# Kernel optimization log

Measured on AMD Instinct MI355X. Metric: run time of the kernel, lower is better.

## Reference

```python
import jax, jax.numpy as jnp
import numpy as np

NUM_COMPONENTS = 8
STRIDE, PADDING, OUTPUT_PADDING, K = 2, 1, 0, 4


def get_comp_mat(n):
    # Cayley-Dickson construction: entry [i, j] = +/- component index of the
    # weight multiplying input component j to produce output component i.
    A = np.array([[0]])
    while A.shape[0] < n:
        m = A.shape[0]
        A = np.vstack([np.hstack([A, -(A + m)]), np.hstack([A + m, A])])
    return A


def setup_inputs() -> dict:
    key = jax.random.key(0)
    k1, k2, k3 = jax.random.split(key, 3)
    B, Cin, Cout, H = 8, 512, 256, 64
    c_in, c_out = Cin // NUM_COMPONENTS, Cout // NUM_COMPONENTS
    x = jax.random.normal(k1, (B, Cin, H, H), jnp.float32)
    # per-component ConvTranspose2d weights, torch layout [C_in, C_out, kH, kW]
    W = jax.random.normal(k2, (NUM_COMPONENTS, c_in, c_out, K, K), jnp.float32) * 0.05
    b = jax.random.normal(k3, (NUM_COMPONENTS, c_out), jnp.float32) * 0.05
    return {"x": x, "W": W, "b": b}


def reference(x, W, b):
    n = NUM_COMPONENTS
    comp = get_comp_mat(n)                 # static [n, n] signed component table
    signs = jnp.asarray(np.where(comp < 0, -1.0, 1.0), x.dtype)
    idx = np.abs(comp)                     # which sub-conv weight to use
    c_in, c_out, kh, kw = W.shape[1:]
    # Fuse the n^2 transpose convs into ONE block transpose conv:
    # Kbig[j*c_in:(j+1)*c_in, i*c_out:(i+1)*c_out] = sign[i,j] * W[idx[i,j]]
    Wsel = W[idx] * signs[:, :, None, None, None, None]          # [ni, nj, c_in, c_out, kh, kw]
    Wbig = jnp.transpose(Wsel, (1, 2, 0, 3, 4, 5)).reshape(n * c_in, n * c_out, kh, kw)
    bbig = jnp.einsum('ij,ijc->ic', signs, b[idx]).reshape(n * c_out)
    # torch ConvTranspose2d == conv with input dilated by stride and flipped kernel
    rhs = jnp.flip(Wbig, (2, 3)).transpose(1, 0, 2, 3)           # OIHW
    pad = K - 1 - PADDING
    out = jax.lax.conv_general_dilated(
        x, rhs, window_strides=(1, 1),
        padding=((pad, pad + OUTPUT_PADDING), (pad, pad + OUTPUT_PADDING)),
        lhs_dilation=(STRIDE, STRIDE),
        dimension_numbers=('NCHW', 'OIHW', 'NCHW'))
    return out + bbig[None, :, None, None]
```

## Files before the change

### kernel.cpp

```cpp
#include <hip/hip_runtime.h>
#include <hip/hip_bf16.h>

typedef unsigned short ushort_t;
typedef __attribute__((ext_vector_type(8))) short short8;
typedef __attribute__((ext_vector_type(4))) float f32x4;

#define NCOMP    8
#define CIN      512
#define COUT     256
#define H        64
#define HP       66
#define OHW      128
#define NB       8

__device__ const int d_idx8[8][8] = {
    {0,1,2,1,4,3,2,3},
    {1,0,3,2,5,4,1,2},
    {2,1,0,1,6,5,4,3},
    {3,2,1,0,7,6,5,4},
    {4,3,2,3,0,1,2,1},
    {5,4,1,2,1,0,3,2},
    {6,5,4,3,2,1,0,1},
    {7,6,5,4,3,2,1,0}};

__device__ const int kh_tab[2][2] = {{1,3},{0,2}};
__device__ const int dh_tab[2][2] = {{0,-1},{1,0}};

__global__ void zero_halo(ushort_t* __restrict__ xpadT) {
    const int t = blockIdx.x * 256 + threadIdx.x;
    const int nA = 8 * 2 * 66 * 64;
    short8 z = {0, 0, 0, 0, 0, 0, 0, 0};
    if (t < nA) {
        int v  = t & 63;
        int r  = t >> 6;
        int iw = r % 66;
        int q  = r / 66;
        int ih = (q & 1) * 65;
        int b  = q >> 1;
        *(short8*)(xpadT + (((size_t)b * HP + ih) * HP + iw) * CIN + v * 8) = z;
    } else {
        int u  = t - nA;
        int v  = u & 63;
        int r  = u >> 6;
        int e  = r & 1;
        int q  = r >> 1;
        int ih = (q & 63) + 1;
        int b  = q >> 6;
        int iw = e * 65;
        *(short8*)(xpadT + (((size_t)b * HP + ih) * HP + iw) * CIN + v * 8) = z;
    }
}

__global__ void prep_x(const float* __restrict__ x, ushort_t* __restrict__ xpadT) {
    __shared__ ushort_t tile[32][33];
    const int ih  = blockIdx.x;
    const int iw0 = (blockIdx.y & 1) * 32;
    const int ic0 = (blockIdx.y >> 1) * 32;
    const int b   = blockIdx.z;
    const int t   = threadIdx.x;

    for (int e = t; e < 1024; e += 256) {
        int icl = e >> 5, iwl = e & 31;
        float v = x[(((size_t)b * CIN + ic0 + icl) * H + ih) * H + iw0 + iwl];
        __hip_bfloat16 h = __float2bfloat16(v);
        tile[icl][iwl] = *(ushort_t*)&h;
    }
    __syncthreads();
    const int iwl = t >> 3, g = t & 7;
    ushort4 v;
    v.x = tile[g * 4 + 0][iwl];
    v.y = tile[g * 4 + 1][iwl];
    v.z = tile[g * 4 + 2][iwl];
    v.w = tile[g * 4 + 3][iwl];
    ushort_t* dst = xpadT + (((size_t)b * HP + ih + 1) * HP + iw0 + iwl + 1) * CIN + ic0 + g * 4;
    *(ushort4*)dst = v;
}

__global__ void prep_w(const float* __restrict__ W, const float* __restrict__ bias,
                       ushort_t* __restrict__ Abf, float* __restrict__ bbig) {
    const int t = blockIdx.x * blockDim.x + threadIdx.x;
    if (t < 4 * 64 * 256 * 32) {
        int kin = t & 31;
        int oc  = (t >> 5) & 255;
        int ks  = (t >> 13) & 63;
        int cls = t >> 19;
        int k  = ks * 32 + kin;
        int a  = k >> 10, c = (k >> 9) & 1, ic = k & 511;
        int ph = cls >> 1, pw = cls & 1;
        int kh = kh_tab[ph][a], kw = kh_tab[pw][c];
        int i = oc >> 5, co = oc & 31;
        int j = ic >> 6, ci = ic & 63;
        float s = (i >= j) ? 1.0f : -1.0f;
        float v = s * W[(((size_t)(d_idx8[i][j] * 64 + ci) * 32 + co) * 4 + kh) * 4 + kw];
        __hip_bfloat16 h = __float2bfloat16(v);
        Abf[t] = *(ushort_t*)&h;
    }
    if (t < COUT) {
        int i = t >> 5, co = t & 31;
        float acc = 0.0f;
        for (int j = 0; j < NCOMP; ++j)
            acc += ((i >= j) ? 1.0f : -1.0f) * bias[d_idx8[i][j] * 32 + co];
        bbig[t] = acc;
    }
}

__device__ __forceinline__ void async16(void* lds_dst, const void* g_src) {
    __builtin_amdgcn_global_load_lds(
        (const __attribute__((address_space(1))) unsigned int*)g_src,
        (__attribute__((address_space(3))) unsigned int*)lds_dst,
        16, 0, 0);
}

#define STAGE(NS, CB)                                                          \
  {                                                                            \
    const int ns_  = (NS);                                                     \
    const int na_  = ns_ >> 5;                                                 \
    const int ncb_ = (ns_ >> 4) & 1;                                           \
    const int go_  = ((na_ ? dh1 : dh0) * HP + (ncb_ ? dw1 : dw0)) * CIN       \
                     + (ns_ & 15) * 32;                                        \
    const ushort_t* nap_ = Abf_t + (size_t)ns_ * 8192;                         \
    async16(sb + (CB) + t * 16,         nap_);                                 \
    async16(sb + (CB) + 4096 + t * 16,  nap_ + 2048);                          \
    async16(sb + (CB) + 8192 + t * 16,  base_r0 + go_);                        \
    async16(sb + (CB) + 12288 + t * 16, base_r1 + go_);                        \
  }

#define COMPUTE(CB)                                                            \
  {                                                                            \
    short8 af[4], bf[4];                                                       \
    _Pragma("unroll")                                                          \
    for (int s = 0; s < 4; ++s) {                                              \
      af[s] = *(const short8*)(sb + (CB) + aoff + s * 1024);                   \
      bf[s] = *(const short8*)(sb + (CB) + boff + s * 1024);                   \
    }                                                                          \
    _Pragma("unroll")                                                          \
    for (int sm = 0; sm < 4; ++sm)                                             \
      _Pragma("unroll")                                                        \
      for (int sn = 0; sn < 4; ++sn)                                           \
        acc[sm][sn] = __builtin_amdgcn_mfma_f32_16x16x32_bf16(                 \
            af[sm], bf[sn], acc[sm][sn], 0, 0, 0);                             \
  }

#define WAITBAR(N)                                                             \
  asm volatile("s_waitcnt vmcnt(" #N ")" ::: "memory");                        \
  __builtin_amdgcn_s_barrier();                                                \
  __builtin_amdgcn_sched_barrier(0);

__launch_bounds__(256)
__global__ void htconv_mfma(const ushort_t* __restrict__ xpadT,
                            const ushort_t* __restrict__ Abf,
                            const float* __restrict__ bbig,
                            float* __restrict__ out) {
    __shared__ __align__(16) ushort_t smem[24576];
    char* sb = (char*)smem;

    const int t     = threadIdx.x;
    const int ntile = blockIdx.x;
    const int mtile = blockIdx.y;
    const int cls   = blockIdx.z & 3;
    const int b     = blockIdx.z >> 2;
    const int ph = cls >> 1, pw = cls & 1;
    const int ohh0 = ntile * 2;

    const int srcc = (((t & 3) ^ ((t >> 3) & 3)) * 8);
    const int m_a  = t >> 2;
    const ushort_t* Abf_t =
        Abf + (((size_t)cls * 64) * 256 + (size_t)mtile * 128 + m_a) * 32 + srcc;

    const int dh0 = dh_tab[ph][0], dh1 = dh_tab[ph][1];
    const int dw0 = dh_tab[pw][0], dw1 = dh_tab[pw][1];
    const int oww = t >> 2;
    const ushort_t* base_r0 =
        xpadT + (((size_t)b * HP + ohh0 + 0 + 1) * HP + oww + 1) * CIN + srcc;
    const ushort_t* base_r1 =
        xpadT + (((size_t)b * HP + ohh0 + 1 + 1) * HP + oww + 1) * CIN + srcc;

    const int lane = t & 63, wave = t >> 6;
    const int wm = wave >> 1, wn = wave & 1;
    const int col = lane & 15, quad = lane >> 4;
    const int soff = (quad ^ ((col >> 1) & 3)) * 16;
    const int aoff = (wm * 64 + col) * 64 + soff;
    const int boff = 8192 + (wn * 64 + col) * 64 + soff;

    f32x4 acc[4][4];
#pragma unroll
    for (int i = 0; i < 4; ++i)
#pragma unroll
        for (int j = 0; j < 4; ++j)
            acc[i][j] = (f32x4){0.f, 0.f, 0.f, 0.f};

    STAGE(0, 0);
    STAGE(1, 16384);

#pragma unroll 1
    for (int i = 0; i < 20; ++i) {
        const int n = 3 * i;
        WAITBAR(4); STAGE(n + 2, 32768); COMPUTE(0);
        WAITBAR(4); STAGE(n + 3, 0);     COMPUTE(16384);
        WAITBAR(4); STAGE(n + 4, 16384); COMPUTE(32768);
    }
    WAITBAR(4); STAGE(62, 32768); COMPUTE(0);
    WAITBAR(4); STAGE(63, 0);     COMPUTE(16384);
    WAITBAR(4);                   COMPUTE(32768);
    WAITBAR(0);                   COMPUTE(0);

    const int oh = 2 * (ohh0 + wn) + ph;
#pragma unroll
    for (int sm = 0; sm < 4; ++sm) {
#pragma unroll
        for (int r = 0; r < 4; ++r) {
            const int occ = mtile * 128 + wm * 64 + sm * 16 + quad * 4 + r;
            const float bv = bbig[occ];
            float* obase = out + (((size_t)b * COUT + occ) * OHW + oh) * OHW + pw;
#pragma unroll
            for (int sn = 0; sn < 4; ++sn) {
                const int owi = sn * 16 + col;
                obase[2 * owi] = acc[sm][sn][r] + bv;
            }
        }
    }
}

extern "C" void kernel_launch(void* const* d_in, const int* in_sizes, int n_in,
                              void* d_out, int out_size, void* d_ws, size_t ws_size,
                              hipStream_t stream) {
    const float* x    = (const float*)d_in[0];
    const float* W    = (const float*)d_in[1];
    const float* bias = (const float*)d_in[2];
    float* out = (float*)d_out;

    ushort_t* xpadT = (ushort_t*)d_ws;
    ushort_t* Abf   = xpadT + (size_t)NB * HP * HP * CIN;
    float*    bbig  = (float*)(Abf + (size_t)4 * 64 * 256 * 32);

    zero_halo<<<dim3(520), 256, 0, stream>>>(xpadT);
    prep_x<<<dim3(H, 32, NB), 256, 0, stream>>>(x, xpadT);
    prep_w<<<dim3((4 * 64 * 256 * 32) / 256), 256, 0, stream>>>(W, bias, Abf, bbig);
    htconv_mfma<<<dim3(32, 2, 32), 256, 0, stream>>>(xpadT, Abf, bbig, out);
}
```

Before: 341.3 us.

## Enlarge GEMM tile to 256x256 with 512-thread blocks and 4-stage pipeline

The block tile grows from 128 output channels x 128 pixels to all 256 channels x 256 pixels (4 output rows), using 512 threads and 8 waves, each holding an 8x4 MFMA accumulator grid. The LDS pipeline moves from 3 stages of 32KB to 4 stages of 32KB (128KB total), and the grid is halved in x with the channel tiles merged. This raises arithmetic intensity and removes duplicate loads of the input across channel tiles. In exchange it roughly doubles accumulator registers, leaves 512 blocks for the device, and the 128KB LDS per block caps occupancy at one block per CU, despite the launch bound asking for two.

```diff
diff --git a/kernel.cpp b/kernel.cpp
--- a/kernel.cpp
+++ b/kernel.cpp
@@ -120,21 +120,22 @@
                      + (ns_ & 15) * 32;                                        \
     const ushort_t* nap_ = Abf_t + (size_t)ns_ * 8192;                         \
     async16(sb + (CB) + t * 16,         nap_);                                 \
-    async16(sb + (CB) + 4096 + t * 16,  nap_ + 2048);                          \
-    async16(sb + (CB) + 8192 + t * 16,  base_r0 + go_);                        \
-    async16(sb + (CB) + 12288 + t * 16, base_r1 + go_);                        \
+    async16(sb + (CB) + 8192 + t * 16,  nap_ + 4096);                          \
+    async16(sb + (CB) + 16384 + t * 16, base_lo + go_);                        \
+    async16(sb + (CB) + 24576 + t * 16, base_hi + go_);                        \
   }
 
 #define COMPUTE(CB)                                                            \
   {                                                                            \
-    short8 af[4], bf[4];                                                       \
+    short8 af[8], bf[4];                                                       \
     _Pragma("unroll")                                                          \
-    for (int s = 0; s < 4; ++s) {                                              \
+    for (int s = 0; s < 8; ++s)                                                \
       af[s] = *(const short8*)(sb + (CB) + aoff + s * 1024);                   \
+    _Pragma("unroll")                                                          \
+    for (int s = 0; s < 4; ++s)                                                \
       bf[s] = *(const short8*)(sb + (CB) + boff + s * 1024);                   \
-    }                                                                          \
     _Pragma("unroll")                                                          \
-    for (int sm = 0; sm < 4; ++sm)                                             \
+    for (int sm = 0; sm < 8; ++sm)                                             \
       _Pragma("unroll")                                                        \
       for (int sn = 0; sn < 4; ++sn)                                           \
         acc[sm][sn] = __builtin_amdgcn_mfma_f32_16x16x32_bf16(                 \
@@ -146,70 +147,70 @@
   __builtin_amdgcn_s_barrier();                                                \
   __builtin_amdgcn_sched_barrier(0);
 
-__launch_bounds__(256)
+__launch_bounds__(512, 2)
 __global__ void htconv_mfma(const ushort_t* __restrict__ xpadT,
                             const ushort_t* __restrict__ Abf,
                             const float* __restrict__ bbig,
                             float* __restrict__ out) {
-    __shared__ __align__(16) ushort_t smem[24576];
+    __shared__ __align__(16) ushort_t smem[65536];
     char* sb = (char*)smem;
 
     const int t     = threadIdx.x;
     const int ntile = blockIdx.x;
-    const int mtile = blockIdx.y;
     const int cls   = blockIdx.z & 3;
     const int b     = blockIdx.z >> 2;
     const int ph = cls >> 1, pw = cls & 1;
-    const int ohh0 = ntile * 2;
+    const int ohh0 = ntile * 4;
 
     const int srcc = (((t & 3) ^ ((t >> 3) & 3)) * 8);
-    const int m_a  = t >> 2;
     const ushort_t* Abf_t =
-        Abf + (((size_t)cls * 64) * 256 + (size_t)mtile * 128 + m_a) * 32 + srcc;
+        Abf + ((size_t)cls * 64) * 8192 + ((size_t)(t >> 2)) * 32 + srcc;
 
     const int dh0 = dh_tab[ph][0], dh1 = dh_tab[ph][1];
     const int dw0 = dh_tab[pw][0], dw1 = dh_tab[pw][1];
-    const int oww = t >> 2;
-    const ushort_t* base_r0 =
-        xpadT + (((size_t)b * HP + ohh0 + 0 + 1) * HP + oww + 1) * CIN + srcc;
-    const ushort_t* base_r1 =
-        xpadT + (((size_t)b * HP + ohh0 + 1 + 1) * HP + oww + 1) * CIN + srcc;
+    const int oww = (t >> 2) & 63;
+    const int rlo = t >> 8;
+    const ushort_t* base_lo =
+        xpadT + (((size_t)b * HP + ohh0 + rlo + 1) * HP + oww + 1) * CIN + srcc;
+    const ushort_t* base_hi = base_lo + (size_t)2 * HP * CIN;
 
     const int lane = t & 63, wave = t >> 6;
-    const int wm = wave >> 1, wn = wave & 1;
+    const int wm = wave >> 2, wn = wave & 3;
     const int col = lane & 15, quad = lane >> 4;
     const int soff = (quad ^ ((col >> 1) & 3)) * 16;
-    const int aoff = (wm * 64 + col) * 64 + soff;
-    const int boff = 8192 + (wn * 64 + col) * 64 + soff;
-
-    f32x4 acc[4][4];
-#pragma unroll
-    for (int i = 0; i < 4; ++i)
+    const int aoff = (wm * 128 + col) * 64 + soff;
+    const int boff = 16384 + (wn * 64 + col) * 64 + soff;
+
+    f32x4 acc[8][4];
+#pragma unroll
+    for (int i = 0; i < 8; ++i)
 #pragma unroll
         for (int j = 0; j < 4; ++j)
             acc[i][j] = (f32x4){0.f, 0.f, 0.f, 0.f};
 
     STAGE(0, 0);
-    STAGE(1, 16384);
+    STAGE(1, 32768);
+    STAGE(2, 65536);
 
 #pragma unroll 1
-    for (int i = 0; i < 20; ++i) {
-        const int n = 3 * i;
-        WAITBAR(4); STAGE(n + 2, 32768); COMPUTE(0);
-        WAITBAR(4); STAGE(n + 3, 0);     COMPUTE(16384);
-        WAITBAR(4); STAGE(n + 4, 16384); COMPUTE(32768);
-    }
-    WAITBAR(4); STAGE(62, 32768); COMPUTE(0);
-    WAITBAR(4); STAGE(63, 0);     COMPUTE(16384);
-    WAITBAR(4);                   COMPUTE(32768);
-    WAITBAR(0);                   COMPUTE(0);
+    for (int i = 0; i < 15; ++i) {
+        const int n = 4 * i;
+        WAITBAR(8); STAGE(n + 3, 98304); COMPUTE(0);
+        WAITBAR(8); STAGE(n + 4, 0);     COMPUTE(32768);
+        WAITBAR(8); STAGE(n + 5, 32768); COMPUTE(65536);
+        WAITBAR(8); STAGE(n + 6, 65536); COMPUTE(98304);
+    }
+    WAITBAR(8); STAGE(63, 98304); COMPUTE(0);
+    WAITBAR(8);                   COMPUTE(32768);
+    WAITBAR(4);                   COMPUTE(65536);
+    WAITBAR(0);                   COMPUTE(98304);
 
     const int oh = 2 * (ohh0 + wn) + ph;
 #pragma unroll
-    for (int sm = 0; sm < 4; ++sm) {
+    for (int sm = 0; sm < 8; ++sm) {
 #pragma unroll
         for (int r = 0; r < 4; ++r) {
-            const int occ = mtile * 128 + wm * 64 + sm * 16 + quad * 4 + r;
+            const int occ = wm * 128 + sm * 16 + quad * 4 + r;
             const float bv = bbig[occ];
             float* obase = out + (((size_t)b * COUT + occ) * OHW + oh) * OHW + pw;
 #pragma unroll
@@ -236,5 +237,5 @@
     zero_halo<<<dim3(520), 256, 0, stream>>>(xpadT);
     prep_x<<<dim3(H, 32, NB), 256, 0, stream>>>(x, xpadT);
     prep_w<<<dim3((4 * 64 * 256 * 32) / 256), 256, 0, stream>>>(W, bias, Abf, bbig);
-    htconv_mfma<<<dim3(32, 2, 32), 256, 0, stream>>>(xpadT, Abf, bbig, out);
-}
+    htconv_mfma<<<dim3(16, 1, 32), 512, 0, stream>>>(xpadT, Abf, bbig, out);
+}
```

New measurement: 313.0 us. -8.3%, faster.
